# Kernel optimization log

Hardware: AMD Instinct MI355X
Metric: run time of the kernel (lower is better)

Reference implementation:

```python
import jax, jax.numpy as jnp
import numpy as np

N_HEAD = 16

def _split_heads(t, n_head):
    B, S, D = t.shape
    return t.reshape(B, S, n_head, D // n_head).transpose(0, 2, 1, 3)  # [B,H,S,dh]

def setup_inputs() -> dict:
    key = jax.random.key(0)
    ks = jax.random.split(key, 12)
    nx = 1024
    B, S, Nv, Nt = 8, 1024, 49, 14
    std = 0.02
    return {
        "x": jax.random.normal(ks[0], (B, S, nx), jnp.float32),
        "visual_features": jax.random.normal(ks[1], (B, Nv, 1024), jnp.float32),
        "tags_embeddings": jax.random.normal(ks[2], (B, Nt, 400), jnp.float32),
        "W_attn": jax.random.normal(ks[3], (nx, 3 * nx), jnp.float32) * std,
        "b_attn": jnp.zeros((3 * nx,), jnp.float32),
        "W_vis": jax.random.normal(ks[4], (1024, 2 * nx), jnp.float32) * std,
        "b_vis": jnp.zeros((2 * nx,), jnp.float32),
        "W_tags": jax.random.normal(ks[5], (400, 2 * nx), jnp.float32) * std,
        "b_tags": jnp.zeros((2 * nx,), jnp.float32),
        "W_proj": jax.random.normal(ks[6], (nx, nx), jnp.float32) * std,
        "b_proj": jnp.zeros((nx,), jnp.float32),
    }

def _forward(x, visual_features, tags_embeddings, W_attn, b_attn, W_vis, b_vis,
             W_tags, b_tags, W_proj, b_proj):
    B, S, nx = x.shape
    H = N_HEAD
    dh = nx // H

    qkv = x @ W_attn + b_attn                       # [B,S,3nx]
    q, k, v = jnp.split(qkv, 3, axis=2)
    q = _split_heads(q, H)                          # [B,H,S,dh]
    k = _split_heads(k, H)
    v = _split_heads(v, H)

    # concat_features(visual): extra keys/values PREPENDED to key/value
    vis = visual_features @ W_vis + b_vis           # [B,Nv,2nx]
    vk, vv = jnp.split(vis, 2, axis=2)
    k = jnp.concatenate([_split_heads(vk, H), k], axis=-2)
    v = jnp.concatenate([_split_heads(vv, H), v], axis=-2)

    # concat_features(tags): prepended in front of [visual, text]
    tg = tags_embeddings @ W_tags + b_tags          # [B,Nt,2nx]
    tk, tv = jnp.split(tg, 2, axis=2)
    k = jnp.concatenate([_split_heads(tk, H), k], axis=-2)
    v = jnp.concatenate([_split_heads(tv, H), v], axis=-2)

    present = jnp.stack([k, v], axis=1)             # [B,2,H,ns,dh]

    nd = S
    ns = k.shape[-2]
    w = jnp.einsum('bhqd,bhkd->bhqk', q, k) / jnp.sqrt(jnp.float32(dh))
    # causal mask counting from lower-right corner: prefix (vis+tags) fully visible
    i = jnp.arange(nd)[:, None]
    j = jnp.arange(ns)[None, :]
    b = (i >= j - ns + nd).astype(w.dtype)          # [nd,ns]
    w = w * b - 10000.0 * (1.0 - b)
    w = jax.nn.softmax(w, axis=-1)

    a = jnp.einsum('bhqk,bhkd->bhqd', w, v)         # [B,H,S,dh]
    a = a.transpose(0, 2, 1, 3).reshape(B, S, nx)   # merge heads
    a = a @ W_proj + b_proj
    return a, present

def reference(x, visual_features, tags_embeddings, W_attn, b_attn, W_vis, b_vis,
              W_tags, b_tags, W_proj, b_proj):
    return _forward(x, visual_features, tags_embeddings, W_attn, b_attn,
                    W_vis, b_vis, W_tags, b_tags, W_proj, b_proj)
```

## Files before the change

### kernel.cpp

```cpp
#include <hip/hip_runtime.h>


typedef __bf16 bf16x8 __attribute__((ext_vector_type(8)));
typedef unsigned short us8 __attribute__((ext_vector_type(8)));
typedef float f32x4 __attribute__((ext_vector_type(4)));

#define NS 1087
#define NSP 1088
#define PFX 63
#define NH 16
#define DH 64
#define SEQ 1024
#define BATCH 8
#define QSCALE 0.18033688011112042f

__device__ __forceinline__ unsigned short f2bf(float f) {
  unsigned int u = __float_as_uint(f);
  u += 0x7fffu + ((u >> 16) & 1u);
  return (unsigned short)(u >> 16);
}

__device__ __forceinline__ us8 cvt8(float4 a, float4 b) {
  us8 r;
  r[0] = f2bf(a.x); r[1] = f2bf(a.y); r[2] = f2bf(a.z); r[3] = f2bf(a.w);
  r[4] = f2bf(b.x); r[5] = f2bf(b.y); r[6] = f2bf(b.z); r[7] = f2bf(b.w);
  return r;
}

__device__ __forceinline__ f32x4 mfma16(us8 a, us8 b, f32x4 c) {
  return __builtin_amdgcn_mfma_f32_16x16x32_bf16(
      __builtin_bit_cast(bf16x8, a), __builtin_bit_cast(bf16x8, b), c, 0, 0, 0);
}

__device__ __forceinline__ void gl2lds16(const void* g, void* l) {
  __builtin_amdgcn_global_load_lds(
      (__attribute__((address_space(1))) void*)(g),
      (__attribute__((address_space(3))) void*)(l), 16, 0, 0);
}

__global__ __launch_bounds__(256) void cvt_bf16_k(
    const float* __restrict__ in, unsigned short* __restrict__ out, int n8) {
  int i = blockIdx.x * 256 + threadIdx.x;
  if (i < n8) {
    const float4* p = (const float4*)in + (size_t)i * 2;
    *(us8*)(out + (size_t)i * 8) = cvt8(p[0], p[1]);
  }
}

__global__ __launch_bounds__(1024) void transpose_cvt_k(
    const float* __restrict__ in, unsigned short* __restrict__ out, int K, int N) {
  __shared__ float tile[32][33];
  const int n0 = blockIdx.x * 32, k0 = blockIdx.y * 32;
  const int tx = threadIdx.x, ty = threadIdx.y;
  tile[ty][tx] = in[(size_t)(k0 + ty) * N + n0 + tx];
  __syncthreads();
  out[(size_t)(n0 + ty) * K + k0 + tx] = f2bf(tile[tx][ty]);
}

__global__ __launch_bounds__(256) void zfill_pad_k(unsigned short* __restrict__ k16) {
  int i = blockIdx.x * 256 + threadIdx.x;
  if (i < BATCH * NH * DH) {
    const int bh = i >> 6, d = i & 63;
    k16[((size_t)bh * NSP + (NSP - 1)) * DH + d] = 0;
  }
}

__global__ __launch_bounds__(256) void vtrans_k(
    const float* __restrict__ present, unsigned short* __restrict__ v16t) {
  __shared__ float tile[64][68];
  const int bh = blockIdx.y;
  const int b = bh >> 4, h = bh & 15;
  const int p0 = blockIdx.x * 64;
  const int t = threadIdx.x;
  const float* src = present + (((size_t)(b * 2 + 1) * NH + h) * NS) * DH;

  const int rr = t >> 2, c0 = (t & 3) * 16;
  const int pos = p0 + rr;
  if (pos < NS) {
    const float4* sp = (const float4*)(src + (size_t)pos * DH + c0);
#pragma unroll
    for (int j = 0; j < 4; ++j) *(float4*)&tile[rr][c0 + 4 * j] = sp[j];
  } else {
    const float4 z = {0.f, 0.f, 0.f, 0.f};
#pragma unroll
    for (int j = 0; j < 4; ++j) *(float4*)&tile[rr][c0 + 4 * j] = z;
  }
  __syncthreads();

  const int d = t >> 2, q0 = (t & 3) * 16;
  us8 o0, o1;
#pragma unroll
  for (int j = 0; j < 8; ++j) {
    o0[j] = f2bf(tile[q0 + j][d]);
    o1[j] = f2bf(tile[q0 + 8 + j][d]);
  }
  unsigned short* dst = v16t + ((size_t)bh * DH + d) * NSP + p0 + q0;
  *(us8*)dst = o0;
  *(us8*)(dst + 8) = o1;
}

template <int MODE>
__global__ __launch_bounds__(256) void gemm128(
    const unsigned short* __restrict__ A, const unsigned short* __restrict__ Bt,
    const float* __restrict__ bias, float* __restrict__ outf,
    float* __restrict__ present, unsigned short* __restrict__ q16,
    unsigned short* __restrict__ k16,
    int M, int N, int K, int nbx) {
  __shared__ unsigned short As[128 * 32];
  __shared__ unsigned short Bs[128 * 32];

  const int bid = blockIdx.x, chunk = gridDim.x >> 3;
  const int wg = (bid & 7) * chunk + (bid >> 3);
  const int bx = wg % nbx, by = wg / nbx;

  const int t = threadIdx.x, w = t >> 6, l = t & 63;
  const int lr = l & 15, lq = l >> 4;
  const int m0 = by * 128, n0 = bx * 128;
  const int wr = (w >> 1) * 64, wc = (w & 1) * 64;

  f32x4 acc[4][4] = {};

  const int arow = w * 32 + (l >> 2);
  const int acol = (l & 3) * 8;
  const unsigned short* gA = A + (size_t)(m0 + arow) * K + acol;
  const unsigned short* gB = Bt + (size_t)(n0 + arow) * K + acol;
  unsigned short* lA0 = As + (w * 32) * 32;
  unsigned short* lA1 = As + (w * 32 + 16) * 32;
  unsigned short* lB0 = Bs + (w * 32) * 32;
  unsigned short* lB1 = Bs + (w * 32 + 16) * 32;

  const int nk = K >> 5;
  for (int kt = 0; kt < nk; ++kt) {
    const size_t ko = (size_t)kt * 32;
    gl2lds16(gA + ko, lA0);
    gl2lds16(gA + (size_t)16 * K + ko, lA1);
    gl2lds16(gB + ko, lB0);
    gl2lds16(gB + (size_t)16 * K + ko, lB1);
    __syncthreads();

    us8 af[4], bfr[4];
#pragma unroll
    for (int i = 0; i < 4; ++i) af[i] = *(us8*)&As[(wr + i * 16 + lr) * 32 + lq * 8];
#pragma unroll
    for (int j = 0; j < 4; ++j) bfr[j] = *(us8*)&Bs[(wc + j * 16 + lr) * 32 + lq * 8];
#pragma unroll
    for (int i = 0; i < 4; ++i)
#pragma unroll
      for (int j = 0; j < 4; ++j)
        acc[i][j] = mfma16(af[i], bfr[j], acc[i][j]);
    __syncthreads();
  }

#pragma unroll
  for (int i = 0; i < 4; ++i) {
    const int row0 = m0 + wr + i * 16 + lq * 4;
#pragma unroll
    for (int j = 0; j < 4; ++j) {
      const int col = n0 + wc + j * 16 + lr;
      const float bv = bias[col];
#pragma unroll
      for (int r = 0; r < 4; ++r) {
        const float v = acc[i][j][r] + bv;
        const int rr = row0 + r;
        if (MODE == 0) {
          outf[(size_t)rr * N + col] = v;
        } else {
          const int b = rr >> 10, s = rr & 1023;
          const int sec = col >> 10, cc = col & 1023, h = cc >> 6, d = cc & 63;
          const int bh = b * NH + h;
          if (sec == 0) {
            q16[((size_t)bh * SEQ + s) * DH + d] = f2bf(v * QSCALE);
          } else {
            const int pos = PFX + s;
            present[(((size_t)(b * 2 + (sec - 1)) * NH + h) * NS + pos) * DH + d] = v;
            if (sec == 1)
              k16[((size_t)bh * NSP + pos) * DH + d] = f2bf(v);
          }
        }
      }
    }
  }
}

template <int MODE>
__global__ __launch_bounds__(256) void gemm64(
    const float* __restrict__ A, const float* __restrict__ W,
    const float* __restrict__ bias, float* __restrict__ present,
    unsigned short* __restrict__ k16,
    int M, int N, int K) {
  __shared__ __align__(16) unsigned short As[64][40];
  __shared__ __align__(16) unsigned short Bs[64][40];

  const int t = threadIdx.x;
  const int m0 = blockIdx.y * 64, n0 = blockIdx.x * 64;
  const int wave = t >> 6, lane = t & 63, lr = lane & 15, lq = lane >> 4;
  const int wr = (wave >> 1) * 32, wc = (wave & 1) * 32;

  f32x4 acc00 = {0,0,0,0}, acc01 = {0,0,0,0}, acc10 = {0,0,0,0}, acc11 = {0,0,0,0};

  const int am = m0 + (t >> 2);
  const int aksub = (t & 3) * 8;
  const int bksub = t >> 3;
  const int bn = n0 + (t & 7) * 8;
  const int nk = (K + 31) / 32;

  for (int kt = 0; kt < nk; ++kt) {
    const int k0 = kt * 32;
    float4 a0 = {0,0,0,0}, a1 = {0,0,0,0};
    const int ak = k0 + aksub;
    if (am < M && ak < K) {
      const float4* ap = (const float4*)(A + (size_t)am * K + ak);
      a0 = ap[0]; a1 = ap[1];
    }
    float4 b0 = {0,0,0,0}, b1 = {0,0,0,0};
    const int bk = k0 + bksub;
    if (bk < K) {
      const float4* bp = (const float4*)(W + (size_t)bk * N + bn);
      b0 = bp[0]; b1 = bp[1];
    }
    __syncthreads();
    *(us8*)&As[t >> 2][aksub] = cvt8(a0, a1);
    {
      unsigned short tmp[8] = {f2bf(b0.x), f2bf(b0.y), f2bf(b0.z), f2bf(b0.w),
                               f2bf(b1.x), f2bf(b1.y), f2bf(b1.z), f2bf(b1.w)};
      const int nn = (t & 7) * 8;
#pragma unroll
      for (int j = 0; j < 8; ++j) Bs[nn + j][bksub] = tmp[j];
    }
    __syncthreads();

    us8 af0 = *(us8*)&As[wr + lr][lq * 8];
    us8 af1 = *(us8*)&As[wr + 16 + lr][lq * 8];
    us8 bf0 = *(us8*)&Bs[wc + lr][lq * 8];
    us8 bf1 = *(us8*)&Bs[wc + 16 + lr][lq * 8];
    acc00 = mfma16(af0, bf0, acc00);
    acc01 = mfma16(af0, bf1, acc01);
    acc10 = mfma16(af1, bf0, acc10);
    acc11 = mfma16(af1, bf1, acc11);
  }

  const int RPB = (MODE == 2) ? 49 : 14;
  const int POFF = (MODE == 2) ? 14 : 0;
  auto store_one = [&](float v, int row, int col) {
    if (row >= M) return;
    v += bias[col];
    const int b = row / RPB, i = row - b * RPB;
    const int sec = col >> 10, cc = col & 1023, h = cc >> 6, d = cc & 63;
    const int pos = POFF + i;
    present[(((size_t)(b * 2 + sec) * NH + h) * NS + pos) * DH + d] = v;
    if (sec == 0)
      k16[((size_t)(b * NH + h) * NSP + pos) * DH + d] = f2bf(v);
  };

#pragma unroll
  for (int r = 0; r < 4; ++r) {
    const int rbase = m0 + wr + lq * 4 + r;
    const int cbase = n0 + wc + lr;
    store_one(acc00[r], rbase,      cbase);
    store_one(acc01[r], rbase,      cbase + 16);
    store_one(acc10[r], rbase + 16, cbase);
    store_one(acc11[r], rbase + 16, cbase + 16);
  }
}

__global__ __launch_bounds__(256) void attn_kernel(
    const unsigned short* __restrict__ q16, const unsigned short* __restrict__ k16,
    const unsigned short* __restrict__ v16t, unsigned short* __restrict__ a16) {
  __shared__ unsigned short Ks[2][64 * 64];
  __shared__ unsigned short Vt[2][64 * 64];
  __shared__ unsigned short Pb[4][16][64];

  const int pair = blockIdx.x >> 7, bh = blockIdx.x & 127;
  const int b = bh >> 4, h = bh & 15;
  const int t = threadIdx.x, w = t >> 6, l = t & 63;
  const int lr = l & 15, lq = l >> 4;

  const unsigned short* Kg = k16 + (size_t)bh * NSP * DH;
  const unsigned short* Vg = v16t + (size_t)bh * DH * NSP;

  const int rsub = l >> 3;
  const int perm = ((l & 7) ^ rsub) << 3;
  const int wrow = w * 16 + rsub;
  const int swr = (lr & 7) << 3;
  int cur = 0;

  for (int seg = 0; seg < 2; ++seg) {
    const int qt = seg ? (15 - pair) : pair;
    const int q0w = qt * 64 + w * 16;

    const unsigned short* qp = q16 + ((size_t)bh * SEQ + q0w + lr) * DH;
    const us8 qa0 = *(const us8*)(qp + lq * 8);
    const us8 qa1 = *(const us8*)(qp + 32 + lq * 8);

    f32x4 o[4] = {};
    float lrow[4] = {0.f, 0.f, 0.f, 0.f};

    gl2lds16(Kg + (size_t)wrow * DH + perm,        Ks[cur] + (w * 16) * 64);
    gl2lds16(Kg + (size_t)(wrow + 8) * DH + perm,  Ks[cur] + (w * 16 + 8) * 64);
    gl2lds16(Vg + (size_t)wrow * NSP + perm,       Vt[cur] + (w * 16) * 64);
    gl2lds16(Vg + (size_t)(wrow + 8) * NSP + perm, Vt[cur] + (w * 16 + 8) * 64);

    const int ntiles = qt + 2;

    for (int kt = 0; kt < ntiles; ++kt) {
      asm volatile("s_waitcnt vmcnt(0)\n\ts_barrier" ::: "memory");
      __builtin_amdgcn_sched_barrier(0);

      if (kt + 1 < ntiles) {
        const int kp1 = (kt + 1) * 64;
        unsigned short* KsN = Ks[cur ^ 1];
        unsigned short* VtN = Vt[cur ^ 1];
        gl2lds16(Kg + (size_t)(kp1 + wrow) * DH + perm,       KsN + (w * 16) * 64);
        gl2lds16(Kg + (size_t)(kp1 + wrow + 8) * DH + perm,   KsN + (w * 16 + 8) * 64);
        gl2lds16(Vg + (size_t)wrow * NSP + kp1 + perm,        VtN + (w * 16) * 64);
        gl2lds16(Vg + (size_t)(wrow + 8) * NSP + kp1 + perm,  VtN + (w * 16 + 8) * 64);
      }

      const unsigned short* KsC = Ks[cur];
      const unsigned short* VtC = Vt[cur];

      f32x4 s[4];
      __builtin_amdgcn_s_setprio(1);
#pragma unroll
      for (int j = 0; j < 4; ++j) {
        const int ro = (j * 16 + lr) * 64;
        const us8 kb0 = *(const us8*)&KsC[ro + ((lq * 8) ^ swr)];
        const us8 kb1 = *(const us8*)&KsC[ro + ((32 + lq * 8) ^ swr)];
        f32x4 z = {};
        z = mfma16(qa0, kb0, z);
        z = mfma16(qa1, kb1, z);
        s[j] = z;
      }
      __builtin_amdgcn_s_setprio(0);

      if (kt == ntiles - 1) {
        const int kp0 = kt * 64;
#pragma unroll
        for (int r = 0; r < 4; ++r) {
          const int lim = q0w + lq * 4 + r + PFX - kp0;
#pragma unroll
          for (int j = 0; j < 4; ++j)
            if (j * 16 + lr > lim) s[j][r] = -1e30f;
        }
      }

#pragma unroll
      for (int r = 0; r < 4; ++r) {
        float p[4];
#pragma unroll
        for (int j = 0; j < 4; ++j) { p[j] = exp2f(s[j][r]); lrow[r] += p[j]; }
        const int prow = lq * 4 + r;
        const int psw = (prow & 7) << 3;
        unsigned short* pb = &Pb[w][prow][0];
#pragma unroll
        for (int j = 0; j < 4; ++j) pb[(j * 16 + lr) ^ psw] = f2bf(p[j]);
      }

      const us8 pf0 = *(const us8*)&Pb[w][lr][(lq * 8) ^ swr];
      const us8 pf1 = *(const us8*)&Pb[w][lr][(32 + lq * 8) ^ swr];
      __builtin_amdgcn_s_setprio(1);
#pragma unroll
      for (int jd = 0; jd < 4; ++jd) {
        const int ro = (jd * 16 + lr) * 64;
        const us8 vb0 = *(const us8*)&VtC[ro + ((lq * 8) ^ swr)];
        const us8 vb1 = *(const us8*)&VtC[ro + ((32 + lq * 8) ^ swr)];
        o[jd] = mfma16(pf0, vb0, o[jd]);
        o[jd] = mfma16(pf1, vb1, o[jd]);
      }
      __builtin_amdgcn_s_setprio(0);
      cur ^= 1;
    }

#pragma unroll
    for (int r = 0; r < 4; ++r) {
      float rs = lrow[r];
      rs += __shfl_xor(rs, 1);
      rs += __shfl_xor(rs, 2);
      rs += __shfl_xor(rs, 4);
      rs += __shfl_xor(rs, 8);
      const float inv = 1.0f / rs;
      const int sr = q0w + lq * 4 + r;
      unsigned short* op = a16 + ((size_t)b * SEQ + sr) * 1024 + h * DH;
#pragma unroll
      for (int jd = 0; jd < 4; ++jd) op[jd * 16 + lr] = f2bf(o[jd][r] * inv);
    }
  }
}

extern "C" void kernel_launch(void* const* d_in, const int* in_sizes, int n_in,
                              void* d_out, int out_size, void* d_ws, size_t ws_size,
                              hipStream_t stream) {
  const float* x      = (const float*)d_in[0];
  const float* vis    = (const float*)d_in[1];
  const float* tags   = (const float*)d_in[2];
  const float* W_attn = (const float*)d_in[3];
  const float* b_attn = (const float*)d_in[4];
  const float* W_vis  = (const float*)d_in[5];
  const float* b_vis  = (const float*)d_in[6];
  const float* W_tags = (const float*)d_in[7];
  const float* b_tags = (const float*)d_in[8];
  const float* W_proj = (const float*)d_in[9];
  const float* b_proj = (const float*)d_in[10];

  float* out_a   = (float*)d_out;
  float* present = out_a + (size_t)BATCH * SEQ * 1024;

  unsigned short* q16 = (unsigned short*)d_out;
  unsigned short* x16 = q16 + (size_t)8192 * 1024;

  char* ws = (char*)d_ws;
  unsigned short* a16   = (unsigned short*)ws;
  unsigned short* wat16 = (unsigned short*)(ws + 16777216);
  unsigned short* wpt16 = (unsigned short*)(ws + 23068672);
  unsigned short* k16   = (unsigned short*)(ws + 25165824);
  unsigned short* v16t  = (unsigned short*)(ws + 42991616);

  const dim3 blk(256);
  zfill_pad_k<<<dim3(32), blk, 0, stream>>>(k16);
  cvt_bf16_k<<<dim3(4096), blk, 0, stream>>>(x, x16, 1048576);
  transpose_cvt_k<<<dim3(96, 32), dim3(32, 32), 0, stream>>>(W_attn, wat16, 1024, 3072);
  transpose_cvt_k<<<dim3(32, 32), dim3(32, 32), 0, stream>>>(W_proj, wpt16, 1024, 1024);
  gemm128<1><<<dim3(1536), blk, 0, stream>>>(
      x16, wat16, b_attn, nullptr, present, q16, k16, 8192, 3072, 1024, 24);
  gemm64<2><<<dim3(2048 / 64, 7), blk, 0, stream>>>(
      vis, W_vis, b_vis, present, k16, 392, 2048, 1024);
  gemm64<3><<<dim3(2048 / 64, 2), blk, 0, stream>>>(
      tags, W_tags, b_tags, present, k16, 112, 2048, 400);
  vtrans_k<<<dim3(17, 128), blk, 0, stream>>>(present, v16t);
  attn_kernel<<<dim3(BATCH * NH * 8), blk, 0, stream>>>(q16, k16, v16t, a16);
  gemm128<0><<<dim3(512), blk, 0, stream>>>(
      a16, wpt16, b_proj, out_a, nullptr, nullptr, nullptr, 8192, 1024, 1024, 8);
}
```

Before: 393.8 us.

## Double-buffer GEMM LDS tiles and XOR-swizzle columns to avoid bank conflicts

The 128x128 GEMM now keeps two LDS buffers for A and B. It issues the global-to-LDS loads for the next k-tile before computing on the current one, and replaces two barriers per iteration with a single waitcnt plus barrier. The column offsets of the LDS tiles are also XOR-swizzled by row so that the fragment reads hit fewer bank conflicts. This doubles LDS use per block, which may lower occupancy.

```diff
diff --git a/kernel.cpp b/kernel.cpp
--- a/kernel.cpp
+++ b/kernel.cpp
@@ -106,8 +106,8 @@
     float* __restrict__ present, unsigned short* __restrict__ q16,
     unsigned short* __restrict__ k16,
     int M, int N, int K, int nbx) {
-  __shared__ unsigned short As[128 * 32];
-  __shared__ unsigned short Bs[128 * 32];
+  __shared__ unsigned short As[2][128 * 32];
+  __shared__ unsigned short Bs[2][128 * 32];
 
   const int bid = blockIdx.x, chunk = gridDim.x >> 3;
   const int wg = (bid & 7) * chunk + (bid >> 3);
@@ -121,34 +121,47 @@
   f32x4 acc[4][4] = {};
 
   const int arow = w * 32 + (l >> 2);
-  const int acol = (l & 3) * 8;
+  const int acol = ((l & 3) ^ ((l >> 3) & 3)) * 8;
   const unsigned short* gA = A + (size_t)(m0 + arow) * K + acol;
   const unsigned short* gB = Bt + (size_t)(n0 + arow) * K + acol;
-  unsigned short* lA0 = As + (w * 32) * 32;
-  unsigned short* lA1 = As + (w * 32 + 16) * 32;
-  unsigned short* lB0 = Bs + (w * 32) * 32;
-  unsigned short* lB1 = Bs + (w * 32 + 16) * 32;
+  const int lo = (w * 32) * 32;
 
   const int nk = K >> 5;
+  {
+    gl2lds16(gA, &As[0][lo]);
+    gl2lds16(gA + (size_t)16 * K, &As[0][lo + 16 * 32]);
+    gl2lds16(gB, &Bs[0][lo]);
+    gl2lds16(gB + (size_t)16 * K, &Bs[0][lo + 16 * 32]);
+  }
+
+  const int csw = ((lr >> 1) & 3) * 8;
+  int cur = 0;
   for (int kt = 0; kt < nk; ++kt) {
-    const size_t ko = (size_t)kt * 32;
-    gl2lds16(gA + ko, lA0);
-    gl2lds16(gA + (size_t)16 * K + ko, lA1);
-    gl2lds16(gB + ko, lB0);
-    gl2lds16(gB + (size_t)16 * K + ko, lB1);
-    __syncthreads();
+    asm volatile("s_waitcnt vmcnt(0)\n\ts_barrier" ::: "memory");
+    __builtin_amdgcn_sched_barrier(0);
+
+    if (kt + 1 < nk) {
+      const size_t ko = (size_t)(kt + 1) * 32;
+      const int nb = cur ^ 1;
+      gl2lds16(gA + ko, &As[nb][lo]);
+      gl2lds16(gA + (size_t)16 * K + ko, &As[nb][lo + 16 * 32]);
+      gl2lds16(gB + ko, &Bs[nb][lo]);
+      gl2lds16(gB + (size_t)16 * K + ko, &Bs[nb][lo + 16 * 32]);
+    }
 
     us8 af[4], bfr[4];
 #pragma unroll
-    for (int i = 0; i < 4; ++i) af[i] = *(us8*)&As[(wr + i * 16 + lr) * 32 + lq * 8];
-#pragma unroll
-    for (int j = 0; j < 4; ++j) bfr[j] = *(us8*)&Bs[(wc + j * 16 + lr) * 32 + lq * 8];
+    for (int i = 0; i < 4; ++i)
+      af[i] = *(us8*)&As[cur][(wr + i * 16 + lr) * 32 + ((lq * 8) ^ csw)];
+#pragma unroll
+    for (int j = 0; j < 4; ++j)
+      bfr[j] = *(us8*)&Bs[cur][(wc + j * 16 + lr) * 32 + ((lq * 8) ^ csw)];
 #pragma unroll
     for (int i = 0; i < 4; ++i)
 #pragma unroll
       for (int j = 0; j < 4; ++j)
         acc[i][j] = mfma16(af[i], bfr[j], acc[i][j]);
-    __syncthreads();
+    cur ^= 1;
   }
 
 #pragma unroll
```

Measured after the change: 381.9 us. -3.0%, faster.
